# Kernel optimization log

Hardware: AMD Instinct MI355X
Metric: run time of the kernel (lower is better)

Reference implementation:

```python
import jax, jax.numpy as jnp
import numpy as np
from itertools import combinations

N_QUBITS = 8
PAIRS = list(combinations(range(N_QUBITS), 2))  # 28 qubit pairs -> 28 features/node

# qubit 0 = first tensor factor (most significant bit of the basis index)
CNOT01 = jnp.array([[1,0,0,0],[0,1,0,0],[0,0,0,1],[0,0,1,0]], dtype=jnp.complex64)  # control q0, target q1
CNOT10 = jnp.array([[1,0,0,0],[0,0,0,1],[0,0,1,0],[0,1,0,0]], dtype=jnp.complex64)  # control q1, target q0
I2 = jnp.eye(2, dtype=jnp.complex64)
HZ = jnp.array([1.0, -1.0, 1.0, -1.0], dtype=jnp.complex64)  # diag(I kron Z)


def _rx(t):
    c = jnp.cos(t / 2).astype(jnp.complex64)
    s = jnp.sin(t / 2).astype(jnp.complex64)
    return jnp.stack([jnp.stack([c, -1j * s]), jnp.stack([-1j * s, c])])


def _ry(t):
    c = jnp.cos(t / 2).astype(jnp.complex64)
    s = jnp.sin(t / 2).astype(jnp.complex64)
    return jnp.stack([jnp.stack([c, -s]), jnp.stack([s, c])])


def _rz(t):
    e = jnp.exp(-0.5j * t.astype(jnp.complex64))
    z = jnp.zeros((), jnp.complex64)
    return jnp.stack([jnp.stack([e, z]), jnp.stack([z, jnp.conj(e)])])


def _pair_unitary(p):  # p: [6] params for one qubit pair
    A = _rz(p[5]) @ _ry(p[4]) @ _rx(p[3]) @ _rz(p[2]) @ _ry(p[1]) @ _rx(p[0])
    return CNOT01 @ (CNOT10 @ jnp.kron(A, I2))  # [4,4]


def _quantum_features(x, qweight):
    """Batched version of the per-node amplitude encoding + 28 two-qubit circuits."""
    N = x.shape[0]
    psi = (x / jnp.linalg.norm(x, axis=1, keepdims=True)).astype(jnp.complex64)  # [N,256]
    psi8 = psi.reshape((N,) + (2,) * N_QUBITS)
    Us = jax.vmap(_pair_unitary)(qweight.reshape(len(PAIRS), 6))  # [28,4,4]
    cols = []
    for p, (a, b) in enumerate(PAIRS):
        perm = (0, 1 + a, 1 + b) + tuple(1 + q for q in range(N_QUBITS) if q not in (a, b))
        v = jnp.transpose(psi8, perm).reshape(N, 4, 2 ** (N_QUBITS - 2))  # [N,4,64]
        rho = jnp.einsum('nim,njm->nij', v, jnp.conj(v))  # reduced 2-qubit DM [N,4,4]
        U = Us[p]
        # <I kron Z> after U rho U^dagger, mapped to [0,1]
        e = jnp.einsum('a,ab,nbc,ac->n', HZ, U, rho, jnp.conj(U))
        cols.append((jnp.real(e) + 1.0) * 0.5)
    return jnp.stack(cols, axis=1).astype(jnp.float32)  # [N,28]


def reference(x, edge_index, qweight, W1, b1, W2, b2):
    N = x.shape[0]
    x_deal = _quantum_features(x, qweight)  # [N,28]
    # gcn_norm with added self loops, edge_weight = 1
    loop = jnp.arange(N)
    src = jnp.concatenate([edge_index[0], loop])
    dst = jnp.concatenate([edge_index[1], loop])
    w = jnp.ones(src.shape[0], dtype=jnp.float32)
    deg = jax.ops.segment_sum(w, dst, num_segments=N)
    dinv = jax.lax.rsqrt(jnp.maximum(deg, 1e-12))
    norm = dinv[src] * w * dinv[dst]
    out = jax.ops.segment_sum(norm[:, None] * x_deal[src], dst, num_segments=N)  # [N,28]
    out = jax.nn.relu(out)
    g = (out.T @ out).reshape(1, 28 * 28)  # [1,784]
    h = jax.nn.relu(g @ W1.T + b1)
    return jax.nn.sigmoid(h @ W2.T + b2)  # [1,1]


def setup_inputs() -> dict:
    N, F, E = 50000, 256, 1600000
    key = jax.random.key(0)
    ks = jax.random.split(key, 6)
    x = jax.random.normal(ks[0], (N, F), dtype=jnp.float32)
    edge_index = jax.random.randint(ks[1], (2, E), 0, N, dtype=jnp.int64)
    qweight = jax.random.uniform(ks[2], (168,), dtype=jnp.float32) * (2.0 * np.pi)
    W1 = jax.random.normal(ks[3], (128, 784), dtype=jnp.float32) * 0.03
    b1 = jnp.zeros((128,), dtype=jnp.float32)
    W2 = jax.random.normal(ks[4], (1, 128), dtype=jnp.float32) * 0.08
    b2 = jnp.zeros((1,), dtype=jnp.float32)
    return {"x": x, "edge_index": edge_index, "qweight": qweight,
            "W1": W1, "b1": b1, "W2": W2, "b2": b2}
```

## Files before the change

kernel.cpp:

```cpp
#include <hip/hip_runtime.h>
#include <hip/hip_fp16.h>
#include <math.h>

#define N_NODES 50000
#define N_EDGES 1600000
#define BSHIFT 6
#define NB_BUCKETS 782
#define PART_CHUNK 8192
#define NCHUNK 196
#define CAP 3072
#define ZSTRIDE 32
#define GREP 16

template<int CTRL>
__device__ inline float dpp_mov(float x){
    return __int_as_float(__builtin_amdgcn_update_dpp(0, __float_as_int(x), CTRL, 0xf, 0xf, false));
}
__device__ inline float wave_sum_dpp(float x){
    x += dpp_mov<0x111>(x);
    x += dpp_mov<0x112>(x);
    x += dpp_mov<0x114>(x);
    x += dpp_mov<0x118>(x);
    x += dpp_mov<0x142>(x);
    x += dpp_mov<0x143>(x);
    return x;
}
__device__ inline float lane63(float x){
    return __int_as_float(__builtin_amdgcn_readlane(__float_as_int(x), 63));
}
#define DPP_XOR1 0xB1
#define DPP_XOR2 0x4E

struct C2 { float x, y; };
__device__ inline C2 mkc(float x, float y){ C2 r; r.x=x; r.y=y; return r; }
__device__ inline C2 cmul(C2 a, C2 b){ return mkc(a.x*b.x - a.y*b.y, a.x*b.y + a.y*b.x); }
__device__ inline C2 cadd(C2 a, C2 b){ return mkc(a.x+b.x, a.y+b.y); }

__global__ __launch_bounds__(256) void k_init(const float* __restrict__ qw,
        const void* __restrict__ ei, float4* __restrict__ cmat,
        int* __restrict__ flag, int* __restrict__ bucketFill, float* __restrict__ G){
    int t = threadIdx.x;
    for (int i = t; i < NB_BUCKETS; i += 256) bucketFill[i] = 0;
    for (int i = t; i < GREP*784; i += 256) G[i] = 0.f;
    if (t == 255){
        const long long* e64 = (const long long*)ei;
        int ok = 1;
        for (int i = 0; i < 64; i++){
            long long v = e64[i];
            if (v < 0 || v >= N_NODES) ok = 0;
        }
        flag[0] = ok;
    }
    if (t < 28){
        int p = t;
        int a = 0; { int rem = p, q = 0; while (rem >= 7 - q){ rem -= 7 - q; q++; } a = q; }
        C2 M00 = mkc(1,0), M01 = mkc(0,0), M10 = mkc(0,0), M11 = mkc(1,0);
        for (int k = 0; k < 6; k++){
            float th = 0.5f * qw[p*6 + k];
            float s, c; sincosf(th, &s, &c);
            C2 R00, R01, R10, R11;
            int type = k % 3;
            if (type == 0){
                R00 = mkc(c,0); R01 = mkc(0,-s); R10 = mkc(0,-s); R11 = mkc(c,0);
            } else if (type == 1){
                R00 = mkc(c,0); R01 = mkc(-s,0); R10 = mkc(s,0); R11 = mkc(c,0);
            } else {
                R00 = mkc(c,-s); R01 = mkc(0,0); R10 = mkc(0,0); R11 = mkc(c,s);
            }
            C2 N00 = cadd(cmul(R00,M00), cmul(R01,M10));
            C2 N01 = cadd(cmul(R00,M01), cmul(R01,M11));
            C2 N10 = cadd(cmul(R10,M00), cmul(R11,M10));
            C2 N11 = cadd(cmul(R10,M01), cmul(R11,M11));
            M00=N00; M01=N01; M10=N10; M11=N11;
        }
        float B00  = (M00.x*M00.x + M00.y*M00.y) - (M10.x*M10.x + M10.y*M10.y);
        float B11  = (M01.x*M01.x + M01.y*M01.y) - (M11.x*M11.x + M11.y*M11.y);
        float B01r = (M00.x*M01.x + M00.y*M01.y) - (M10.x*M11.x + M10.y*M11.y);
        cmat[p] = make_float4(0.5f + 0.5f*B11, 0.5f*(B00 - B11), B01r, (float)a);
    }
}

__device__ inline int get_edge(const void* ei, int is64, long long idx){
    if (is64) return (int)((const long long*)ei)[idx];
    return ((const int*)ei)[idx];
}

__global__ __launch_bounds__(1024) void k_part(const void* __restrict__ ei,
        const int* __restrict__ flag, int* __restrict__ bucketFill,
        unsigned* __restrict__ pairs){
    __shared__ int hist[NB_BUCKETS];
    __shared__ int cntb[NB_BUCKETS];
    __shared__ int cursor[NB_BUCKETS];
    __shared__ int copyBase[NB_BUCKETS];
    __shared__ unsigned sorted[PART_CHUNK];
    int tid = threadIdx.x, c = blockIdx.x;
    long long base = (long long)c * PART_CHUNK;
    int cnt = (int)((N_EDGES - base < PART_CHUNK) ? (N_EDGES - base) : PART_CHUNK);
    int is64 = flag[0];
    unsigned ds[8], sr[8];
    #pragma unroll
    for (int k = 0; k < 8; k++){
        int i = tid + 1024*k;
        if (i < cnt){
            ds[k] = (unsigned)get_edge(ei, is64, (long long)N_EDGES + base + i);
            sr[k] = (unsigned)get_edge(ei, is64, base + i);
        } else ds[k] = 0xffffffffu;
    }
    if (tid < NB_BUCKETS) hist[tid] = 0;
    __syncthreads();
    #pragma unroll
    for (int k = 0; k < 8; k++)
        if (ds[k] != 0xffffffffu) atomicAdd(&hist[ds[k] >> BSHIFT], 1);
    __syncthreads();
    if (tid < NB_BUCKETS) cntb[tid] = hist[tid];
    __syncthreads();
    for (int ofs = 1; ofs < NB_BUCKETS; ofs <<= 1){
        int v = 0; bool a = tid < NB_BUCKETS;
        if (a) v = hist[tid] + (tid >= ofs ? hist[tid - ofs] : 0);
        __syncthreads();
        if (a) hist[tid] = v;
        __syncthreads();
    }
    if (tid < NB_BUCKETS){
        int cb = cntb[tid];
        int ls = hist[tid] - cb;
        int gbase = tid*CAP + atomicAdd(&bucketFill[tid], cb);
        copyBase[tid] = gbase - ls;
        cursor[tid] = ls;
    }
    __syncthreads();
    #pragma unroll
    for (int k = 0; k < 8; k++){
        if (ds[k] != 0xffffffffu){
            int pos = atomicAdd(&cursor[ds[k] >> BSHIFT], 1);
            sorted[pos] = (ds[k] << 16) | sr[k];
        }
    }
    __syncthreads();
    for (int i = tid; i < cnt; i += 1024){
        unsigned v = sorted[i];
        int b = (int)(v >> 22);
        pairs[copyBase[b] + i] = v;
    }
}

__global__ __launch_bounds__(256) void k_deg(const unsigned* __restrict__ pairs,
        const int* __restrict__ bucketFill, float* __restrict__ dinv){
    __shared__ int hist[64];
    int b = blockIdx.x, t = threadIdx.x;
    int s0 = b*CAP;
    int cnt = bucketFill[b];
    if (cnt > CAP) cnt = CAP;
    if (t < 64) hist[t] = 0;
    __syncthreads();
    for (int i = t; i < cnt; i += 256)
        atomicAdd(&hist[(pairs[s0 + i] >> 16) & 63], 1);
    __syncthreads();
    if (t < 64){
        int n = b*64 + t;
        if (n < N_NODES) dinv[n] = rsqrtf((float)(hist[t] + 1));
    }
}

__global__ __launch_bounds__(256) void k_feat(const float* __restrict__ x,
        const float* __restrict__ dinv, const float4* __restrict__ cmat,
        __half* __restrict__ z){
    int wave = threadIdx.x >> 6;
    int lane = threadIdx.x & 63;
    int n = blockIdx.x*4 + wave;
    const float4 v = ((const float4*)(x + (size_t)n*256))[lane];
    float persq = v.x*v.x + v.y*v.y + v.z*v.z + v.w*v.w;

    float red[15];
    red[0] = persq;
    red[1] = v.x*v.x + v.y*v.y;
    red[2] = v.x*v.z + v.y*v.w;
    {
        float px = dpp_mov<DPP_XOR1>(v.x), py = dpp_mov<DPP_XOR1>(v.y);
        float pz = dpp_mov<DPP_XOR1>(v.z), pw = dpp_mov<DPP_XOR1>(v.w);
        red[3] = v.x*px + v.y*py + v.z*pz + v.w*pw;
        red[9] = (lane & 1) ? 0.f : persq;
    }
    {
        float px = dpp_mov<DPP_XOR2>(v.x), py = dpp_mov<DPP_XOR2>(v.y);
        float pz = dpp_mov<DPP_XOR2>(v.z), pw = dpp_mov<DPP_XOR2>(v.w);
        red[4] = v.x*px + v.y*py + v.z*pz + v.w*pw;
        red[10] = (lane & 2) ? 0.f : persq;
    }
    #pragma unroll
    for (int j = 2; j < 6; j++){
        float px = __shfl_xor(v.x, 1 << j), py = __shfl_xor(v.y, 1 << j);
        float pz = __shfl_xor(v.z, 1 << j), pw = __shfl_xor(v.w, 1 << j);
        red[3 + j] = v.x*px + v.y*py + v.z*pz + v.w*pw;
        red[9 + j] = ((lane >> j) & 1) ? 0.0f : persq;
    }
    float S[15];
    #pragma unroll
    for (int k = 0; k < 15; k++) S[k] = lane63(wave_sum_dpp(red[k]));

    if (lane < 28){
        float4 cm = cmat[lane];
        int ap = (int)cm.w;
        float S0a = (ap==6) ? S[1] :
                    (ap==0 ? S[14] : ap==1 ? S[13] : ap==2 ? S[12] :
                     ap==3 ? S[11] : ap==4 ? S[10] : S[9]);
        float Xa  = (ap==6) ? S[2] :
                    0.5f*(ap==0 ? S[8] : ap==1 ? S[7] : ap==2 ? S[6] :
                          ap==3 ? S[5] : ap==4 ? S[4] : S[3]);
        float feat = cm.x + (cm.y*S0a + cm.z*Xa) / S[0];
        z[(size_t)n*ZSTRIDE + lane] = __float2half(dinv[n] * feat);
    } else if (lane < 32){
        z[(size_t)n*ZSTRIDE + lane] = __float2half(0.f);
    }
}

__device__ inline void acc_pack(unsigned u, float& a, float& b){
    float2 f = __half22float2(__builtin_bit_cast(__half2, u));
    a += f.x; b += f.y;
}
__device__ inline void acc_row(const uint4* rp, float* acc ){
    uint4 w0 = rp[0], w1 = rp[1], w2 = rp[2], w3 = rp[3];
    acc_pack(w0.x, acc[0],  acc[1]);  acc_pack(w0.y, acc[2],  acc[3]);
    acc_pack(w0.z, acc[4],  acc[5]);  acc_pack(w0.w, acc[6],  acc[7]);
    acc_pack(w1.x, acc[8],  acc[9]);  acc_pack(w1.y, acc[10], acc[11]);
    acc_pack(w1.z, acc[12], acc[13]); acc_pack(w1.w, acc[14], acc[15]);
    acc_pack(w2.x, acc[16], acc[17]); acc_pack(w2.y, acc[18], acc[19]);
    acc_pack(w2.z, acc[20], acc[21]); acc_pack(w2.w, acc[22], acc[23]);
    acc_pack(w3.x, acc[24], acc[25]); acc_pack(w3.y, acc[26], acc[27]);
    acc_pack(w3.z, acc[28], acc[29]); acc_pack(w3.w, acc[30], acc[31]);
}

__global__ __launch_bounds__(512) void k_bucket(const unsigned* __restrict__ pairs,
        const int* __restrict__ bucketFill, const __half* __restrict__ z,
        const float* __restrict__ dinv, float* __restrict__ G){
    __shared__ unsigned short sorted[CAP];
    __shared__ int hist[64];
    __shared__ int cursor[64];
    __shared__ int begs[64];
    __shared__ int cnts[64];
    __shared__ float srow[64*28];
    int b = blockIdx.x, t = threadIdx.x;
    int s0 = b*CAP;
    int cnt = bucketFill[b];
    if (cnt > CAP) cnt = CAP;
    if (t < 64) hist[t] = 0;
    __syncthreads();
    for (int i = t; i < cnt; i += 512){
        unsigned v = pairs[s0 + i];
        atomicAdd(&hist[(v >> 16) & 63], 1);
    }
    __syncthreads();
    int mycnt = (t < 64) ? hist[t] : 0;
    for (int ofs = 1; ofs < 64; ofs <<= 1){
        int nv = 0;
        if (t < 64) nv = hist[t] + (t >= ofs ? hist[t - ofs] : 0);
        __syncthreads();
        if (t < 64) hist[t] = nv;
        __syncthreads();
    }
    if (t < 64){
        cursor[t] = hist[t] - mycnt;
        begs[t]   = hist[t] - mycnt;
        cnts[t]   = mycnt;
    }
    __syncthreads();
    for (int i = t; i < cnt; i += 512){
        unsigned v = pairs[s0 + i];
        int d = (v >> 16) & 63;
        int pos = atomicAdd(&cursor[d], 1);
        sorted[pos] = (unsigned short)(v & 0xffffu);
    }
    __syncthreads();

    int d = t >> 3, sub = t & 7;
    int n = b*64 + d;
    bool valid = n < N_NODES;
    float acc[32];
    #pragma unroll
    for (int k = 0; k < 32; k++) acc[k] = 0.f;
    if (valid){
        int beg = begs[d], end = beg + cnts[d];
        for (int i = beg + sub; i < end; i += 8){
            int src = sorted[i];
            acc_row((const uint4*)(z + (size_t)src*ZSTRIDE), acc);
        }
        if (sub == 7) acc_row((const uint4*)(z + (size_t)n*ZSTRIDE), acc);
    }
    #pragma unroll
    for (int k = 0; k < 32; k++){
        acc[k] += dpp_mov<DPP_XOR1>(acc[k]);
        acc[k] += dpp_mov<DPP_XOR2>(acc[k]);
        acc[k] += __shfl_xor(acc[k], 4);
    }
    if (sub == 0){
        float dv = valid ? dinv[n] : 0.f;
        #pragma unroll
        for (int k = 0; k < 28; k++)
            srow[d*28 + k] = fmaxf(acc[k]*dv, 0.f);
    }
    __syncthreads();

    if (t < 196){
        float* Gr = G + (size_t)(blockIdx.x & (GREP-1)) * 784;
        int ti = t / 14, tj = t % 14;
        int i0 = 2*ti, j0 = 2*tj;
        float c00 = 0.f, c01 = 0.f, c10 = 0.f, c11 = 0.f;
        for (int nn = 0; nn < 64; nn++){
            const float* r = srow + nn*28;
            float a0 = r[i0], a1 = r[i0+1], b0 = r[j0], b1 = r[j0+1];
            c00 += a0*b0; c01 += a0*b1; c10 += a1*b0; c11 += a1*b1;
        }
        atomicAdd(&Gr[(i0  )*28 + j0  ], c00);
        atomicAdd(&Gr[(i0  )*28 + j0+1], c01);
        atomicAdd(&Gr[(i0+1)*28 + j0  ], c10);
        atomicAdd(&Gr[(i0+1)*28 + j0+1], c11);
    }
}

__global__ __launch_bounds__(256) void k_mlp(const float* __restrict__ G,
        const float* __restrict__ W1, const float* __restrict__ b1,
        const float* __restrict__ W2, const float* __restrict__ b2,
        float* __restrict__ outp){
    __shared__ float Gs[784];
    __shared__ float part[256];
    __shared__ float h[128];
    int t = threadIdx.x;
    for (int i = t; i < 784; i += 256){
        float s = 0.f;
        #pragma unroll
        for (int r = 0; r < GREP; r++) s += G[r*784 + i];
        Gs[i] = s;
    }
    __syncthreads();
    int j = t & 127, halfsel = t >> 7;
    const float* w = W1 + (size_t)j*784 + halfsel*392;
    const float* g = Gs + halfsel*392;
    float s = 0.f;
    for (int i = 0; i < 392; i++) s += g[i] * w[i];
    part[t] = s;
    __syncthreads();
    if (t < 128) h[t] = fmaxf(part[t] + part[t+128] + b1[t], 0.f) * W2[t];
    __syncthreads();
    for (int ofs = 64; ofs > 0; ofs >>= 1){
        if (t < ofs) h[t] += h[t + ofs];
        __syncthreads();
    }
    if (t == 0) outp[0] = 1.f / (1.f + expf(-(h[0] + b2[0])));
}

extern "C" void kernel_launch(void* const* d_in, const int* in_sizes, int n_in,
                              void* d_out, int out_size, void* d_ws, size_t ws_size,
                              hipStream_t stream){
    const float* x  = (const float*)d_in[0];
    const void*  ei = d_in[1];
    const float* qw = (const float*)d_in[2];
    const float* W1 = (const float*)d_in[3];
    const float* b1 = (const float*)d_in[4];
    const float* W2 = (const float*)d_in[5];
    const float* b2 = (const float*)d_in[6];
    float* outp = (float*)d_out;

    char* base = (char*)d_ws;
    __half*         z     = (__half*)base;         base += (size_t)N_NODES*ZSTRIDE*2;
    unsigned*       pairs = (unsigned*)base;       base += (size_t)NB_BUCKETS*CAP*4;
    float*          dinv  = (float*)base;          base += (size_t)N_NODES*4;
    float4*         cmat  = (float4*)base;         base += 448;
    float*          G     = (float*)base;          base += GREP*784*4;
    int*            bucketFill = (int*)base;       base += 4096;
    int*            flag  = (int*)base;            base += 16;

    k_init<<<1, 256, 0, stream>>>(qw, ei, cmat, flag, bucketFill, G);
    k_part<<<NCHUNK, 1024, 0, stream>>>(ei, flag, bucketFill, pairs);
    k_deg<<<NB_BUCKETS, 256, 0, stream>>>(pairs, bucketFill, dinv);
    k_feat<<<N_NODES/4, 256, 0, stream>>>(x, dinv, cmat, z);
    k_bucket<<<NB_BUCKETS, 512, 0, stream>>>(pairs, bucketFill, z, dinv, G);
    k_mlp<<<1, 256, 0, stream>>>(G, W1, b1, W2, b2, outp);
}
```

Measured before the change: 176.4 us.

## Fuse all stages into one cooperative persistent kernel with grid syncs

```diff
diff --git a/kernel.cpp b/kernel.cpp
--- a/kernel.cpp
+++ b/kernel.cpp
@@ -1,16 +1,22 @@
 #include <hip/hip_runtime.h>
 #include <hip/hip_fp16.h>
+#include <hip/hip_cooperative_groups.h>
 #include <math.h>
+
+namespace cg = cooperative_groups;
 
 #define N_NODES 50000
 #define N_EDGES 1600000
 #define BSHIFT 6
 #define NB_BUCKETS 782
-#define PART_CHUNK 8192
-#define NCHUNK 196
+#define NBLK 256
+#define NTHR 1024
+#define PART_CHUNK 6250
+#define EPT 7
 #define CAP 3072
 #define ZSTRIDE 32
 #define GREP 16
+#define DEG_BLOCKS 64
 
 template<int CTRL>
 __device__ inline float dpp_mov(float x){
@@ -36,22 +42,57 @@
 __device__ inline C2 cmul(C2 a, C2 b){ return mkc(a.x*b.x - a.y*b.y, a.x*b.y + a.y*b.x); }
 __device__ inline C2 cadd(C2 a, C2 b){ return mkc(a.x+b.x, a.y+b.y); }
 
-__global__ __launch_bounds__(256) void k_init(const float* __restrict__ qw,
-        const void* __restrict__ ei, float4* __restrict__ cmat,
-        int* __restrict__ flag, int* __restrict__ bucketFill, float* __restrict__ G){
-    int t = threadIdx.x;
-    for (int i = t; i < NB_BUCKETS; i += 256) bucketFill[i] = 0;
-    for (int i = t; i < GREP*784; i += 256) G[i] = 0.f;
-    if (t == 255){
-        const long long* e64 = (const long long*)ei;
-        int ok = 1;
-        for (int i = 0; i < 64; i++){
-            long long v = e64[i];
-            if (v < 0 || v >= N_NODES) ok = 0;
-        }
-        flag[0] = ok;
-    }
-    if (t < 28){
+__device__ inline int get_edge(const void* ei, int is64, long long idx){
+    if (is64) return (int)((const long long*)ei)[idx];
+    return ((const int*)ei)[idx];
+}
+
+__device__ inline void acc_pack(unsigned u, float w, float& a, float& b){
+    float2 f = __half22float2(__builtin_bit_cast(__half2, u));
+    a = fmaf(w, f.x, a); b = fmaf(w, f.y, b);
+}
+__device__ inline void acc_row(float w, const uint4* rp, float* acc ){
+    uint4 w0 = rp[0], w1 = rp[1], w2 = rp[2], w3 = rp[3];
+    acc_pack(w0.x, w, acc[0],  acc[1]);  acc_pack(w0.y, w, acc[2],  acc[3]);
+    acc_pack(w0.z, w, acc[4],  acc[5]);  acc_pack(w0.w, w, acc[6],  acc[7]);
+    acc_pack(w1.x, w, acc[8],  acc[9]);  acc_pack(w1.y, w, acc[10], acc[11]);
+    acc_pack(w1.z, w, acc[12], acc[13]); acc_pack(w1.w, w, acc[14], acc[15]);
+    acc_pack(w2.x, w, acc[16], acc[17]); acc_pack(w2.y, w, acc[18], acc[19]);
+    acc_pack(w2.z, w, acc[20], acc[21]); acc_pack(w2.w, w, acc[22], acc[23]);
+    acc_pack(w3.x, w, acc[24], acc[25]); acc_pack(w3.y, w, acc[26], acc[27]);
+    acc_pack(w3.z, w, acc[28], acc[29]); acc_pack(w3.w, w, acc[30], acc[31]);
+}
+
+struct PartS {
+    int hist[NB_BUCKETS]; int cntb[NB_BUCKETS];
+    int cursor[NB_BUCKETS]; int copyBase[NB_BUCKETS];
+    unsigned sorted[PART_CHUNK];
+};
+struct BucketS {
+    unsigned short sorted[CAP];
+    int hist[64]; int cursor[64]; int begs[64]; int cnts[64];
+    float srow[64*28];
+};
+struct MlpS { float Gs[784]; float prt[NTHR]; float h[128]; };
+union SMem { PartS part; BucketS bucket; MlpS mlp; };
+
+__global__ __launch_bounds__(NTHR, 4) void k_mega(
+        const float* __restrict__ x, const void* __restrict__ ei,
+        const float* __restrict__ qw, const float* __restrict__ W1,
+        const float* __restrict__ b1, const float* __restrict__ W2,
+        const float* __restrict__ b2, float* __restrict__ outp,
+        __half* __restrict__ z, unsigned* __restrict__ pairs,
+        float* __restrict__ dinv, float4* __restrict__ cmat,
+        float* __restrict__ G, int* __restrict__ bucketFill)
+{
+    __shared__ SMem U;
+    __shared__ int is64_s;
+    cg::grid_group grid = cg::this_grid();
+    const int t = threadIdx.x, blk = blockIdx.x;
+
+    for (int i = blk*NTHR + t; i < GREP*784; i += NBLK*NTHR) G[i] = 0.f;
+    for (int i = blk*NTHR + t; i < NB_BUCKETS; i += NBLK*NTHR) bucketFill[i] = 0;
+    if (blk == 0 && t < 28){
         int p = t;
         int a = 0; { int rem = p, q = 0; while (rem >= 7 - q){ rem -= 7 - q; q++; } a = q; }
         C2 M00 = mkc(1,0), M01 = mkc(0,0), M10 = mkc(0,0), M11 = mkc(1,0);
@@ -78,274 +119,242 @@
         float B01r = (M00.x*M01.x + M00.y*M01.y) - (M10.x*M11.x + M10.y*M11.y);
         cmat[p] = make_float4(0.5f + 0.5f*B11, 0.5f*(B00 - B11), B01r, (float)a);
     }
-}
-
-__device__ inline int get_edge(const void* ei, int is64, long long idx){
-    if (is64) return (int)((const long long*)ei)[idx];
-    return ((const int*)ei)[idx];
-}
-
-__global__ __launch_bounds__(1024) void k_part(const void* __restrict__ ei,
-        const int* __restrict__ flag, int* __restrict__ bucketFill,
-        unsigned* __restrict__ pairs){
-    __shared__ int hist[NB_BUCKETS];
-    __shared__ int cntb[NB_BUCKETS];
-    __shared__ int cursor[NB_BUCKETS];
-    __shared__ int copyBase[NB_BUCKETS];
-    __shared__ unsigned sorted[PART_CHUNK];
-    int tid = threadIdx.x, c = blockIdx.x;
-    long long base = (long long)c * PART_CHUNK;
-    int cnt = (int)((N_EDGES - base < PART_CHUNK) ? (N_EDGES - base) : PART_CHUNK);
-    int is64 = flag[0];
-    unsigned ds[8], sr[8];
-    #pragma unroll
-    for (int k = 0; k < 8; k++){
-        int i = tid + 1024*k;
-        if (i < cnt){
-            ds[k] = (unsigned)get_edge(ei, is64, (long long)N_EDGES + base + i);
-            sr[k] = (unsigned)get_edge(ei, is64, base + i);
-        } else ds[k] = 0xffffffffu;
-    }
-    if (tid < NB_BUCKETS) hist[tid] = 0;
-    __syncthreads();
-    #pragma unroll
-    for (int k = 0; k < 8; k++)
-        if (ds[k] != 0xffffffffu) atomicAdd(&hist[ds[k] >> BSHIFT], 1);
-    __syncthreads();
-    if (tid < NB_BUCKETS) cntb[tid] = hist[tid];
-    __syncthreads();
-    for (int ofs = 1; ofs < NB_BUCKETS; ofs <<= 1){
-        int v = 0; bool a = tid < NB_BUCKETS;
-        if (a) v = hist[tid] + (tid >= ofs ? hist[tid - ofs] : 0);
-        __syncthreads();
-        if (a) hist[tid] = v;
-        __syncthreads();
-    }
-    if (tid < NB_BUCKETS){
-        int cb = cntb[tid];
-        int ls = hist[tid] - cb;
-        int gbase = tid*CAP + atomicAdd(&bucketFill[tid], cb);
-        copyBase[tid] = gbase - ls;
-        cursor[tid] = ls;
-    }
-    __syncthreads();
-    #pragma unroll
-    for (int k = 0; k < 8; k++){
-        if (ds[k] != 0xffffffffu){
-            int pos = atomicAdd(&cursor[ds[k] >> BSHIFT], 1);
-            sorted[pos] = (ds[k] << 16) | sr[k];
-        }
-    }
-    __syncthreads();
-    for (int i = tid; i < cnt; i += 1024){
-        unsigned v = sorted[i];
-        int b = (int)(v >> 22);
-        pairs[copyBase[b] + i] = v;
-    }
-}
-
-__global__ __launch_bounds__(256) void k_deg(const unsigned* __restrict__ pairs,
-        const int* __restrict__ bucketFill, float* __restrict__ dinv){
-    __shared__ int hist[64];
-    int b = blockIdx.x, t = threadIdx.x;
-    int s0 = b*CAP;
-    int cnt = bucketFill[b];
-    if (cnt > CAP) cnt = CAP;
-    if (t < 64) hist[t] = 0;
-    __syncthreads();
-    for (int i = t; i < cnt; i += 256)
-        atomicAdd(&hist[(pairs[s0 + i] >> 16) & 63], 1);
-    __syncthreads();
-    if (t < 64){
-        int n = b*64 + t;
-        if (n < N_NODES) dinv[n] = rsqrtf((float)(hist[t] + 1));
-    }
-}
-
-__global__ __launch_bounds__(256) void k_feat(const float* __restrict__ x,
-        const float* __restrict__ dinv, const float4* __restrict__ cmat,
-        __half* __restrict__ z){
-    int wave = threadIdx.x >> 6;
-    int lane = threadIdx.x & 63;
-    int n = blockIdx.x*4 + wave;
-    const float4 v = ((const float4*)(x + (size_t)n*256))[lane];
-    float persq = v.x*v.x + v.y*v.y + v.z*v.z + v.w*v.w;
-
-    float red[15];
-    red[0] = persq;
-    red[1] = v.x*v.x + v.y*v.y;
-    red[2] = v.x*v.z + v.y*v.w;
+    grid.sync();
+
     {
-        float px = dpp_mov<DPP_XOR1>(v.x), py = dpp_mov<DPP_XOR1>(v.y);
-        float pz = dpp_mov<DPP_XOR1>(v.z), pw = dpp_mov<DPP_XOR1>(v.w);
-        red[3] = v.x*px + v.y*py + v.z*pz + v.w*pw;
-        red[9] = (lane & 1) ? 0.f : persq;
-    }
-    {
-        float px = dpp_mov<DPP_XOR2>(v.x), py = dpp_mov<DPP_XOR2>(v.y);
-        float pz = dpp_mov<DPP_XOR2>(v.z), pw = dpp_mov<DPP_XOR2>(v.w);
-        red[4] = v.x*px + v.y*py + v.z*pz + v.w*pw;
-        red[10] = (lane & 2) ? 0.f : persq;
-    }
-    #pragma unroll
-    for (int j = 2; j < 6; j++){
-        float px = __shfl_xor(v.x, 1 << j), py = __shfl_xor(v.y, 1 << j);
-        float pz = __shfl_xor(v.z, 1 << j), pw = __shfl_xor(v.w, 1 << j);
-        red[3 + j] = v.x*px + v.y*py + v.z*pz + v.w*pw;
-        red[9 + j] = ((lane >> j) & 1) ? 0.0f : persq;
-    }
-    float S[15];
-    #pragma unroll
-    for (int k = 0; k < 15; k++) S[k] = lane63(wave_sum_dpp(red[k]));
-
-    if (lane < 28){
-        float4 cm = cmat[lane];
-        int ap = (int)cm.w;
-        float S0a = (ap==6) ? S[1] :
-                    (ap==0 ? S[14] : ap==1 ? S[13] : ap==2 ? S[12] :
-                     ap==3 ? S[11] : ap==4 ? S[10] : S[9]);
-        float Xa  = (ap==6) ? S[2] :
-                    0.5f*(ap==0 ? S[8] : ap==1 ? S[7] : ap==2 ? S[6] :
-                          ap==3 ? S[5] : ap==4 ? S[4] : S[3]);
-        float feat = cm.x + (cm.y*S0a + cm.z*Xa) / S[0];
-        z[(size_t)n*ZSTRIDE + lane] = __float2half(dinv[n] * feat);
-    } else if (lane < 32){
-        z[(size_t)n*ZSTRIDE + lane] = __float2half(0.f);
-    }
-}
-
-__device__ inline void acc_pack(unsigned u, float& a, float& b){
-    float2 f = __half22float2(__builtin_bit_cast(__half2, u));
-    a += f.x; b += f.y;
-}
-__device__ inline void acc_row(const uint4* rp, float* acc ){
-    uint4 w0 = rp[0], w1 = rp[1], w2 = rp[2], w3 = rp[3];
-    acc_pack(w0.x, acc[0],  acc[1]);  acc_pack(w0.y, acc[2],  acc[3]);
-    acc_pack(w0.z, acc[4],  acc[5]);  acc_pack(w0.w, acc[6],  acc[7]);
-    acc_pack(w1.x, acc[8],  acc[9]);  acc_pack(w1.y, acc[10], acc[11]);
-    acc_pack(w1.z, acc[12], acc[13]); acc_pack(w1.w, acc[14], acc[15]);
-    acc_pack(w2.x, acc[16], acc[17]); acc_pack(w2.y, acc[18], acc[19]);
-    acc_pack(w2.z, acc[20], acc[21]); acc_pack(w2.w, acc[22], acc[23]);
-    acc_pack(w3.x, acc[24], acc[25]); acc_pack(w3.y, acc[26], acc[27]);
-    acc_pack(w3.z, acc[28], acc[29]); acc_pack(w3.w, acc[30], acc[31]);
-}
-
-__global__ __launch_bounds__(512) void k_bucket(const unsigned* __restrict__ pairs,
-        const int* __restrict__ bucketFill, const __half* __restrict__ z,
-        const float* __restrict__ dinv, float* __restrict__ G){
-    __shared__ unsigned short sorted[CAP];
-    __shared__ int hist[64];
-    __shared__ int cursor[64];
-    __shared__ int begs[64];
-    __shared__ int cnts[64];
-    __shared__ float srow[64*28];
-    int b = blockIdx.x, t = threadIdx.x;
-    int s0 = b*CAP;
-    int cnt = bucketFill[b];
-    if (cnt > CAP) cnt = CAP;
-    if (t < 64) hist[t] = 0;
-    __syncthreads();
-    for (int i = t; i < cnt; i += 512){
-        unsigned v = pairs[s0 + i];
-        atomicAdd(&hist[(v >> 16) & 63], 1);
-    }
-    __syncthreads();
-    int mycnt = (t < 64) ? hist[t] : 0;
-    for (int ofs = 1; ofs < 64; ofs <<= 1){
-        int nv = 0;
-        if (t < 64) nv = hist[t] + (t >= ofs ? hist[t - ofs] : 0);
-        __syncthreads();
-        if (t < 64) hist[t] = nv;
-        __syncthreads();
-    }
-    if (t < 64){
-        cursor[t] = hist[t] - mycnt;
-        begs[t]   = hist[t] - mycnt;
-        cnts[t]   = mycnt;
-    }
-    __syncthreads();
-    for (int i = t; i < cnt; i += 512){
-        unsigned v = pairs[s0 + i];
-        int d = (v >> 16) & 63;
-        int pos = atomicAdd(&cursor[d], 1);
-        sorted[pos] = (unsigned short)(v & 0xffffu);
-    }
-    __syncthreads();
-
-    int d = t >> 3, sub = t & 7;
-    int n = b*64 + d;
-    bool valid = n < N_NODES;
-    float acc[32];
-    #pragma unroll
-    for (int k = 0; k < 32; k++) acc[k] = 0.f;
-    if (valid){
-        int beg = begs[d], end = beg + cnts[d];
-        for (int i = beg + sub; i < end; i += 8){
-            int src = sorted[i];
-            acc_row((const uint4*)(z + (size_t)src*ZSTRIDE), acc);
-        }
-        if (sub == 7) acc_row((const uint4*)(z + (size_t)n*ZSTRIDE), acc);
-    }
-    #pragma unroll
-    for (int k = 0; k < 32; k++){
-        acc[k] += dpp_mov<DPP_XOR1>(acc[k]);
-        acc[k] += dpp_mov<DPP_XOR2>(acc[k]);
-        acc[k] += __shfl_xor(acc[k], 4);
-    }
-    if (sub == 0){
-        float dv = valid ? dinv[n] : 0.f;
-        #pragma unroll
-        for (int k = 0; k < 28; k++)
-            srow[d*28 + k] = fmaxf(acc[k]*dv, 0.f);
-    }
-    __syncthreads();
-
-    if (t < 196){
-        float* Gr = G + (size_t)(blockIdx.x & (GREP-1)) * 784;
-        int ti = t / 14, tj = t % 14;
-        int i0 = 2*ti, j0 = 2*tj;
-        float c00 = 0.f, c01 = 0.f, c10 = 0.f, c11 = 0.f;
-        for (int nn = 0; nn < 64; nn++){
-            const float* r = srow + nn*28;
-            float a0 = r[i0], a1 = r[i0+1], b0 = r[j0], b1 = r[j0+1];
-            c00 += a0*b0; c01 += a0*b1; c10 += a1*b0; c11 += a1*b1;
-        }
-        atomicAdd(&Gr[(i0  )*28 + j0  ], c00);
-        atomicAdd(&Gr[(i0  )*28 + j0+1], c01);
-        atomicAdd(&Gr[(i0+1)*28 + j0  ], c10);
-        atomicAdd(&Gr[(i0+1)*28 + j0+1], c11);
-    }
-}
-
-__global__ __launch_bounds__(256) void k_mlp(const float* __restrict__ G,
-        const float* __restrict__ W1, const float* __restrict__ b1,
-        const float* __restrict__ W2, const float* __restrict__ b2,
-        float* __restrict__ outp){
-    __shared__ float Gs[784];
-    __shared__ float part[256];
-    __shared__ float h[128];
-    int t = threadIdx.x;
-    for (int i = t; i < 784; i += 256){
+        if (t == 0) is64_s = 1;
+        __syncthreads();
+        if (t < 64){
+            long long v = ((const long long*)ei)[t];
+            if (v < 0 || v >= N_NODES) atomicAnd(&is64_s, 0);
+        }
+        __syncthreads();
+        int is64 = is64_s;
+        long long base = (long long)blk * PART_CHUNK;
+        const int cnt = PART_CHUNK;
+        unsigned ds[EPT], sr[EPT];
+        #pragma unroll
+        for (int k = 0; k < EPT; k++){
+            int i = t + NTHR*k;
+            if (i < cnt){
+                ds[k] = (unsigned)get_edge(ei, is64, (long long)N_EDGES + base + i);
+                sr[k] = (unsigned)get_edge(ei, is64, base + i);
+            } else ds[k] = 0xffffffffu;
+        }
+        if (t < NB_BUCKETS) U.part.hist[t] = 0;
+        __syncthreads();
+        #pragma unroll
+        for (int k = 0; k < EPT; k++)
+            if (ds[k] != 0xffffffffu) atomicAdd(&U.part.hist[ds[k] >> BSHIFT], 1);
+        __syncthreads();
+        if (t < NB_BUCKETS) U.part.cntb[t] = U.part.hist[t];
+        __syncthreads();
+        for (int ofs = 1; ofs < NB_BUCKETS; ofs <<= 1){
+            int v = 0; bool a = t < NB_BUCKETS;
+            if (a) v = U.part.hist[t] + (t >= ofs ? U.part.hist[t - ofs] : 0);
+            __syncthreads();
+            if (a) U.part.hist[t] = v;
+            __syncthreads();
+        }
+        if (t < NB_BUCKETS){
+            int cb = U.part.cntb[t];
+            int ls = U.part.hist[t] - cb;
+            int gbase = t*CAP + atomicAdd(&bucketFill[t], cb);
+            U.part.copyBase[t] = gbase - ls;
+            U.part.cursor[t] = ls;
+        }
+        __syncthreads();
+        #pragma unroll
+        for (int k = 0; k < EPT; k++){
+            if (ds[k] != 0xffffffffu){
+                int pos = atomicAdd(&U.part.cursor[ds[k] >> BSHIFT], 1);
+                U.part.sorted[pos] = (ds[k] << 16) | sr[k];
+            }
+        }
+        __syncthreads();
+        for (int i = t; i < cnt; i += NTHR){
+            unsigned v = U.part.sorted[i];
+            int b = (int)(v >> 22);
+            pairs[U.part.copyBase[b] + i] = v;
+        }
+    }
+    grid.sync();
+
+    if (blk < DEG_BLOCKS){
+        for (int vb = blk; vb < NB_BUCKETS; vb += DEG_BLOCKS){
+            if (t < 64) U.bucket.hist[t] = 0;
+            __syncthreads();
+            int s0 = vb*CAP;
+            int cnt = bucketFill[vb]; if (cnt > CAP) cnt = CAP;
+            for (int i = t; i < cnt; i += NTHR)
+                atomicAdd(&U.bucket.hist[(pairs[s0 + i] >> 16) & 63], 1);
+            __syncthreads();
+            if (t < 64){
+                int n = vb*64 + t;
+                if (n < N_NODES) dinv[n] = rsqrtf((float)(U.bucket.hist[t] + 1));
+            }
+            __syncthreads();
+        }
+    } else {
+        int wv = t >> 6, lane = t & 63;
+        int wid = (blk - DEG_BLOCKS)*16 + wv;
+        const int WSTRIDE = (NBLK - DEG_BLOCKS)*16;
+        for (int n = wid; n < N_NODES; n += WSTRIDE){
+            const float4 v = ((const float4*)(x + (size_t)n*256))[lane];
+            float persq = v.x*v.x + v.y*v.y + v.z*v.z + v.w*v.w;
+            float red[15];
+            red[0] = persq;
+            red[1] = v.x*v.x + v.y*v.y;
+            red[2] = v.x*v.z + v.y*v.w;
+            {
+                float px = dpp_mov<DPP_XOR1>(v.x), py = dpp_mov<DPP_XOR1>(v.y);
+                float pz = dpp_mov<DPP_XOR1>(v.z), pw = dpp_mov<DPP_XOR1>(v.w);
+                red[3] = v.x*px + v.y*py + v.z*pz + v.w*pw;
+                red[9] = (lane & 1) ? 0.f : persq;
+            }
+            {
+                float px = dpp_mov<DPP_XOR2>(v.x), py = dpp_mov<DPP_XOR2>(v.y);
+                float pz = dpp_mov<DPP_XOR2>(v.z), pw = dpp_mov<DPP_XOR2>(v.w);
+                red[4] = v.x*px + v.y*py + v.z*pz + v.w*pw;
+                red[10] = (lane & 2) ? 0.f : persq;
+            }
+            #pragma unroll
+            for (int j = 2; j < 6; j++){
+                float px = __shfl_xor(v.x, 1 << j), py = __shfl_xor(v.y, 1 << j);
+                float pz = __shfl_xor(v.z, 1 << j), pw = __shfl_xor(v.w, 1 << j);
+                red[3 + j] = v.x*px + v.y*py + v.z*pz + v.w*pw;
+                red[9 + j] = ((lane >> j) & 1) ? 0.0f : persq;
+            }
+            float S[15];
+            #pragma unroll
+            for (int k = 0; k < 15; k++) S[k] = lane63(wave_sum_dpp(red[k]));
+            if (lane < 28){
+                float4 cm = cmat[lane];
+                int ap = (int)cm.w;
+                float S0a = (ap==6) ? S[1] :
+                            (ap==0 ? S[14] : ap==1 ? S[13] : ap==2 ? S[12] :
+                             ap==3 ? S[11] : ap==4 ? S[10] : S[9]);
+                float Xa  = (ap==6) ? S[2] :
+                            0.5f*(ap==0 ? S[8] : ap==1 ? S[7] : ap==2 ? S[6] :
+                                  ap==3 ? S[5] : ap==4 ? S[4] : S[3]);
+                float feat = cm.x + (cm.y*S0a + cm.z*Xa) / S[0];
+                z[(size_t)n*ZSTRIDE + lane] = __float2half(feat);
+            } else if (lane < 32){
+                z[(size_t)n*ZSTRIDE + lane] = __float2half(0.f);
+            }
+        }
+    }
+    grid.sync();
+
+    for (int vb = blk; vb < NB_BUCKETS; vb += NBLK){
+        int s0 = vb*CAP;
+        int cnt = bucketFill[vb]; if (cnt > CAP) cnt = CAP;
+        if (t < 64) U.bucket.hist[t] = 0;
+        __syncthreads();
+        for (int i = t; i < cnt; i += NTHR){
+            unsigned v = pairs[s0 + i];
+            atomicAdd(&U.bucket.hist[(v >> 16) & 63], 1);
+        }
+        __syncthreads();
+        int mycnt = (t < 64) ? U.bucket.hist[t] : 0;
+        for (int ofs = 1; ofs < 64; ofs <<= 1){
+            int nv = 0;
+            if (t < 64) nv = U.bucket.hist[t] + (t >= ofs ? U.bucket.hist[t - ofs] : 0);
+            __syncthreads();
+            if (t < 64) U.bucket.hist[t] = nv;
+            __syncthreads();
+        }
+        if (t < 64){
+            U.bucket.cursor[t] = U.bucket.hist[t] - mycnt;
+            U.bucket.begs[t]   = U.bucket.hist[t] - mycnt;
+            U.bucket.cnts[t]   = mycnt;
+        }
+        __syncthreads();
+        for (int i = t; i < cnt; i += NTHR){
+            unsigned v = pairs[s0 + i];
+            int d = (v >> 16) & 63;
+            int pos = atomicAdd(&U.bucket.cursor[d], 1);
+            U.bucket.sorted[pos] = (unsigned short)(v & 0xffffu);
+        }
+        __syncthreads();
+
+        int d = t >> 4, sub = t & 15;
+        int n = vb*64 + d;
+        bool valid = n < N_NODES;
+        float acc[32];
+        #pragma unroll
+        for (int k = 0; k < 32; k++) acc[k] = 0.f;
+        if (valid){
+            int beg = U.bucket.begs[d], end = beg + U.bucket.cnts[d];
+            for (int i = beg + sub; i < end; i += 16){
+                int src = U.bucket.sorted[i];
+                acc_row(dinv[src], (const uint4*)(z + (size_t)src*ZSTRIDE), acc);
+            }
+            if (sub == 15)
+                acc_row(dinv[n], (const uint4*)(z + (size_t)n*ZSTRIDE), acc);
+        }
+        #pragma unroll
+        for (int k = 0; k < 32; k++){
+            acc[k] += dpp_mov<DPP_XOR1>(acc[k]);
+            acc[k] += dpp_mov<DPP_XOR2>(acc[k]);
+            acc[k] += __shfl_xor(acc[k], 4);
+            acc[k] += __shfl_xor(acc[k], 8);
+        }
+        if (sub == 0){
+            float dv = valid ? dinv[n] : 0.f;
+            #pragma unroll
+            for (int k = 0; k < 28; k++)
+                U.bucket.srow[d*28 + k] = fmaxf(acc[k]*dv, 0.f);
+        }
+        __syncthreads();
+
+        if (t < 196){
+            float* Gr = G + (size_t)(vb & (GREP-1)) * 784;
+            int ti = t / 14, tj = t % 14;
+            int i0 = 2*ti, j0 = 2*tj;
+            float c00 = 0.f, c01 = 0.f, c10 = 0.f, c11 = 0.f;
+            for (int nn = 0; nn < 64; nn++){
+                const float* r = U.bucket.srow + nn*28;
+                float a0 = r[i0], a1 = r[i0+1], b0 = r[j0], b1 = r[j0+1];
+                c00 += a0*b0; c01 += a0*b1; c10 += a1*b0; c11 += a1*b1;
+            }
+            atomicAdd(&Gr[(i0  )*28 + j0  ], c00);
+            atomicAdd(&Gr[(i0  )*28 + j0+1], c01);
+            atomicAdd(&Gr[(i0+1)*28 + j0  ], c10);
+            atomicAdd(&Gr[(i0+1)*28 + j0+1], c11);
+        }
+        __syncthreads();
+    }
+    grid.sync();
+
+    if (blk == 0){
+        for (int i = t; i < 784; i += NTHR){
+            float s = 0.f;
+            #pragma unroll
+            for (int r = 0; r < GREP; r++) s += G[r*784 + i];
+            U.mlp.Gs[i] = s;
+        }
+        __syncthreads();
+        int j = t & 127, q = t >> 7;
+        const float* w = W1 + (size_t)j*784 + q*98;
+        const float* g = U.mlp.Gs + q*98;
         float s = 0.f;
-        #pragma unroll
-        for (int r = 0; r < GREP; r++) s += G[r*784 + i];
-        Gs[i] = s;
-    }
-    __syncthreads();
-    int j = t & 127, halfsel = t >> 7;
-    const float* w = W1 + (size_t)j*784 + halfsel*392;
-    const float* g = Gs + halfsel*392;
-    float s = 0.f;
-    for (int i = 0; i < 392; i++) s += g[i] * w[i];
-    part[t] = s;
-    __syncthreads();
-    if (t < 128) h[t] = fmaxf(part[t] + part[t+128] + b1[t], 0.f) * W2[t];
-    __syncthreads();
-    for (int ofs = 64; ofs > 0; ofs >>= 1){
-        if (t < ofs) h[t] += h[t + ofs];
-        __syncthreads();
-    }
-    if (t == 0) outp[0] = 1.f / (1.f + expf(-(h[0] + b2[0])));
+        for (int i = 0; i < 98; i++) s += g[i] * w[i];
+        U.mlp.prt[t] = s;
+        __syncthreads();
+        if (t < 128){
+            float hv = b1[t];
+            #pragma unroll
+            for (int qq = 0; qq < 8; qq++) hv += U.mlp.prt[t + 128*qq];
+            U.mlp.h[t] = fmaxf(hv, 0.f) * W2[t];
+        }
+        __syncthreads();
+        for (int ofs = 64; ofs > 0; ofs >>= 1){
+            if (t < ofs) U.mlp.h[t] += U.mlp.h[t + ofs];
+            __syncthreads();
+        }
+        if (t == 0) outp[0] = 1.f / (1.f + expf(-(U.mlp.h[0] + b2[0])));
+    }
 }
 
 extern "C" void kernel_launch(void* const* d_in, const int* in_sizes, int n_in,
@@ -361,18 +370,16 @@
     float* outp = (float*)d_out;
 
     char* base = (char*)d_ws;
-    __half*         z     = (__half*)base;         base += (size_t)N_NODES*ZSTRIDE*2;
-    unsigned*       pairs = (unsigned*)base;       base += (size_t)NB_BUCKETS*CAP*4;
-    float*          dinv  = (float*)base;          base += (size_t)N_NODES*4;
-    float4*         cmat  = (float4*)base;         base += 448;
-    float*          G     = (float*)base;          base += GREP*784*4;
-    int*            bucketFill = (int*)base;       base += 4096;
-    int*            flag  = (int*)base;            base += 16;
-
-    k_init<<<1, 256, 0, stream>>>(qw, ei, cmat, flag, bucketFill, G);
-    k_part<<<NCHUNK, 1024, 0, stream>>>(ei, flag, bucketFill, pairs);
-    k_deg<<<NB_BUCKETS, 256, 0, stream>>>(pairs, bucketFill, dinv);
-    k_feat<<<N_NODES/4, 256, 0, stream>>>(x, dinv, cmat, z);
-    k_bucket<<<NB_BUCKETS, 512, 0, stream>>>(pairs, bucketFill, z, dinv, G);
-    k_mlp<<<1, 256, 0, stream>>>(G, W1, b1, W2, b2, outp);
-}
+    __half*   z     = (__half*)base;   base += (size_t)N_NODES*ZSTRIDE*2;
+    unsigned* pairs = (unsigned*)base; base += (size_t)NB_BUCKETS*CAP*4;
+    float*    dinv  = (float*)base;    base += (size_t)N_NODES*4;
+    float4*   cmat  = (float4*)base;   base += 448;
+    float*    G     = (float*)base;    base += GREP*784*4;
+    int*      bucketFill = (int*)base; base += 4096;
+
+    void* kargs[] = { (void*)&x, (void*)&ei, (void*)&qw, (void*)&W1, (void*)&b1,
+                      (void*)&W2, (void*)&b2, (void*)&outp, (void*)&z, (void*)&pairs,
+                      (void*)&dinv, (void*)&cmat, (void*)&G, (void*)&bucketFill };
+    hipLaunchCooperativeKernel((const void*)k_mega, dim3(NBLK), dim3(NTHR),
+                               kargs, 0, stream);
+}
```

Result: slower. 324.1 us (+83.8%).
